# Kernel tuning notes

Hardware: AMD Instinct MI355X
Metric: run time of the kernel (lower is better)

The kernel has to match this reference:

```python
import jax, jax.numpy as jnp
import numpy as np
import math

B, S, D, H = 4, 2048, 1024, 16
HD = D // H  # head_dim = 64


def setup_inputs() -> dict:
    key = jax.random.key(0)
    ks = jax.random.split(key, 12)
    inv = 1.0 / math.sqrt(D)
    inp = {
        "query": jax.random.normal(ks[0], (B, S, D), dtype=jnp.float32),
        "key": jax.random.normal(ks[1], (B, S, D), dtype=jnp.float32),
        "value": jax.random.normal(ks[2], (B, S, D), dtype=jnp.float32),
        # causal mask, broadcast over heads; guarantees no all-masked softmax rows
        "mask": jnp.tril(jnp.ones((S, S), dtype=jnp.int32))[None, None].repeat(B, axis=0),
        # linear params stored as (in, out); y = x @ W + b (same math as torch Linear)
        "Wq": jax.random.uniform(ks[3], (D, D), jnp.float32, -inv, inv),
        "bq": jax.random.uniform(ks[4], (D,), jnp.float32, -inv, inv),
        "Wk": jax.random.uniform(ks[5], (D, D), jnp.float32, -inv, inv),
        "bk": jax.random.uniform(ks[6], (D,), jnp.float32, -inv, inv),
        "Wv": jax.random.uniform(ks[7], (D, D), jnp.float32, -inv, inv),
        "bv": jax.random.uniform(ks[8], (D,), jnp.float32, -inv, inv),
        "Wo": jax.random.uniform(ks[9], (D, D), jnp.float32, -inv, inv),
        "bo": jax.random.uniform(ks[10], (D,), jnp.float32, -inv, inv),
    }
    return inp


def _split_heads(x):
    # [B, S, D] -> [B, H, S, HD]
    b, s, _ = x.shape
    return x.reshape(b, s, H, HD).transpose(0, 2, 1, 3)


def reference(query, key, value, mask, Wq, bq, Wk, bk, Wv, bv, Wo, bo):
    q = _split_heads(query @ Wq + bq)   # [B,H,S,HD]
    k = _split_heads(key @ Wk + bk)
    v = _split_heads(value @ Wv + bv)
    scores = jnp.einsum("bhqd,bhkd->bhqk", q, k)          # [B,H,S,S]
    scores = jnp.where(mask == 0, -jnp.inf, scores)
    attn = jax.nn.softmax(scores / math.sqrt(HD), axis=-1)
    attn = attn * mask.astype(attn.dtype)                  # post-softmax re-mask (as in source)
    out = jnp.einsum("bhqk,bhkd->bhqd", attn, v)           # [B,H,S,HD]
    out = out.transpose(0, 2, 1, 3).reshape(query.shape[0], -1, D)
    return out @ Wo + bo
```

## Files before the change

### kernel.cpp

```cpp
#include <hip/hip_runtime.h>

typedef __attribute__((ext_vector_type(8))) short short8;
typedef __attribute__((ext_vector_type(8))) unsigned short ushort8;
typedef __attribute__((ext_vector_type(4))) unsigned short us4;
typedef __attribute__((ext_vector_type(4))) float f32x4;
typedef __attribute__((ext_vector_type(4))) int i32x4;

#define S_LEN 2048
#define D_MODEL 1024
#define N_HEADS 16
#define HEAD_DIM 64

__device__ __forceinline__ unsigned short f2bf(float f) {
  union { float f; unsigned u; } x; x.f = f;
  unsigned r = x.u + 0x7FFFu + ((x.u >> 16) & 1u);
  return (unsigned short)(r >> 16);
}

__device__ __forceinline__ int pkbf(float a, float b) {
  union { float f; unsigned u; } x, y;
  x.f = a; y.f = b;
  return (int)__builtin_amdgcn_perm(y.u + 0x8000u, x.u + 0x8000u, 0x07060302u);
}

__global__ __launch_bounds__(256) void cvt3_kernel(const float* __restrict__ a,
                                                   const float* __restrict__ b,
                                                   const float* __restrict__ c,
                                                   unsigned short* __restrict__ oa,
                                                   unsigned short* __restrict__ ob,
                                                   unsigned short* __restrict__ oc) {
  int bid = blockIdx.x;
  const float* in = (bid < 4096) ? a : (bid < 8192 ? b : c);
  unsigned short* out = (bid < 4096) ? oa : (bid < 8192 ? ob : oc);
  int i = (bid & 4095) * 256 + threadIdx.x;
  const f32x4* in4 = (const f32x4*)in;
  f32x4 x = in4[2 * i], y = in4[2 * i + 1];
  i32x4 o;
  o[0] = pkbf(x[0], x[1]);
  o[1] = pkbf(x[2], x[3]);
  o[2] = pkbf(y[0], y[1]);
  o[3] = pkbf(y[2], y[3]);
  ((i32x4*)out)[i] = o;
}

__global__ __launch_bounds__(256) void transpose_w4(
    const float* __restrict__ Wq, const float* __restrict__ Wk,
    const float* __restrict__ Wv, const float* __restrict__ Wo,
    unsigned short* __restrict__ wqkvT, unsigned short* __restrict__ woT) {
  __shared__ float tile[64][65];
  const int z = blockIdx.z;
  const float* W = (z == 0) ? Wq : (z == 1) ? Wk : (z == 2) ? Wv : Wo;
  unsigned short* Wt = (z < 3) ? (wqkvT + (size_t)z * D_MODEL * D_MODEL) : woT;
  const int no = blockIdx.x * 64, ko = blockIdx.y * 64;
  const int tx = threadIdx.x & 63, ty = threadIdx.x >> 6;
  for (int r = ty; r < 64; r += 4)
    tile[r][tx] = W[(size_t)(ko + r) * D_MODEL + no + tx];
  __syncthreads();
  for (int r = ty; r < 64; r += 4)
    Wt[(size_t)(no + r) * D_MODEL + ko + tx] = f2bf(tile[tx][r]);
}

template <int MODE>
__global__ __launch_bounds__(256) void proj_gemm(
    const unsigned short* __restrict__ A0,
    const unsigned short* __restrict__ A1,
    const unsigned short* __restrict__ A2,
    const unsigned short* __restrict__ Bt,
    const float* __restrict__ b0p, const float* __restrict__ b1p,
    const float* __restrict__ b2p,
    void* __restrict__ o0, void* __restrict__ o1, void* __restrict__ o2,
    float qscale) {
  __shared__ __align__(16) unsigned short sm[16384];
  unsigned short* As = sm;
  unsigned short* Bs = sm + 8192;
  const int tid = threadIdx.x;
  const int wave = tid >> 6, lane = tid & 63;
  const int quad = lane >> 4, l16 = lane & 15;

  const int nlin = blockIdx.y * (MODE == 0 ? 24 : 8) + blockIdx.x;
  const int xcd = nlin & 7;
  const int j = nlin >> 3;
  int bx_eff, by_eff;
  if (MODE == 0) {
    by_eff = xcd * 8 + ((j & 63) >> 3);
    bx_eff = (j >> 6) * 8 + (j & 7);
  } else {
    by_eff = xcd * 8 + (j >> 3);
    bx_eff = j & 7;
  }
  const int m0 = by_eff * 128, n0 = bx_eff * 128;
  const int wm = (wave >> 1) * 64, wn = (wave & 1) * 64;

  const int sel = (MODE == 0) ? (n0 >> 10) : 0;
  const unsigned short* A = (MODE == 0) ? (sel == 0 ? A0 : sel == 1 ? A1 : A2) : A0;
  const float* bias = (MODE == 0) ? (sel == 0 ? b0p : sel == 1 ? b1p : b2p) : b0p;
  const float scale = (MODE == 0 && sel == 0) ? qscale : 1.0f;
  const int nb = (MODE == 0) ? (n0 & 1023) : n0;

  f32x4 acc[4][4] = {};

  int grow[4], gcol[4];
  for (int i = 0; i < 4; ++i) {
    int cid = (wave * 4 + i) * 64 + lane;
    int r = cid >> 3;
    grow[i] = r;
    gcol[i] = ((cid & 7) ^ (r & 7)) * 8;
  }

  for (int k0 = 0; k0 < D_MODEL; k0 += 64) {
#pragma unroll
    for (int i = 0; i < 4; ++i) {
      const unsigned short* g = A + (size_t)(m0 + grow[i]) * D_MODEL + k0 + gcol[i];
      __builtin_amdgcn_global_load_lds((const __attribute__((address_space(1))) void*)g,
          (__attribute__((address_space(3))) void*)(As + (wave * 4 + i) * 512), 16, 0, 0);
    }
#pragma unroll
    for (int i = 0; i < 4; ++i) {
      const unsigned short* g = Bt + (size_t)(n0 + grow[i]) * D_MODEL + k0 + gcol[i];
      __builtin_amdgcn_global_load_lds((const __attribute__((address_space(1))) void*)g,
          (__attribute__((address_space(3))) void*)(Bs + (wave * 4 + i) * 512), 16, 0, 0);
    }
    __syncthreads();
#pragma unroll
    for (int t = 0; t < 2; ++t) {
      short8 af[4], bf[4];
#pragma unroll
      for (int i = 0; i < 4; ++i) {
        int r = wm + i * 16 + l16;
        af[i] = *(const short8*)(As + r * 64 + (((t * 4 + quad) ^ (r & 7)) << 3));
      }
#pragma unroll
      for (int j2 = 0; j2 < 4; ++j2) {
        int r = wn + j2 * 16 + l16;
        bf[j2] = *(const short8*)(Bs + r * 64 + (((t * 4 + quad) ^ (r & 7)) << 3));
      }
#pragma unroll
      for (int i = 0; i < 4; ++i)
#pragma unroll
        for (int j2 = 0; j2 < 4; ++j2)
          acc[i][j2] = __builtin_amdgcn_mfma_f32_16x16x32_bf16(af[i], bf[j2], acc[i][j2], 0, 0, 0);
    }
    __syncthreads();
  }

  float bv4[4];
#pragma unroll
  for (int j2 = 0; j2 < 4; ++j2) bv4[j2] = bias[nb + wn + j2 * 16 + l16];

  if (MODE == 0) {
    if (sel < 2) {
      unsigned short* T = As + wave * 1152;
      unsigned short* out = (unsigned short*)(sel == 0 ? o0 : o1);
      const int h = (nb + wn) >> 6;
#pragma unroll
      for (int i = 0; i < 4; ++i) {
#pragma unroll
        for (int j2 = 0; j2 < 4; ++j2)
#pragma unroll
          for (int r = 0; r < 4; ++r)
            T[(quad * 4 + r) * 72 + j2 * 16 + l16] = f2bf((acc[i][j2][r] + bv4[j2]) * scale);
        int m = m0 + wm + i * 16 + l16;
        int b = m >> 11, s = m & 2047;
#pragma unroll
        for (int t = 0; t < 2; ++t) {
          short8 row = *(const short8*)(T + l16 * 72 + t * 32 + quad * 8);
          *(short8*)(out + (((size_t)(b * N_HEADS + h) * S_LEN + s) << 6) + t * 32 + quad * 8) = row;
        }
      }
    } else {
      unsigned short* vt = (unsigned short*)o2;
#pragma unroll
      for (int i = 0; i < 4; ++i) {
        int m = m0 + wm + i * 16 + quad * 4;
        int b = m >> 11, s = m & 2047;
#pragma unroll
        for (int j2 = 0; j2 < 4; ++j2) {
          int n = nb + wn + j2 * 16 + l16;
          int h = n >> 6, d = n & 63;
          us4 pv;
#pragma unroll
          for (int r = 0; r < 4; ++r) pv[r] = f2bf(acc[i][j2][r] + bv4[j2]);
          *(us4*)(vt + (((size_t)(b * N_HEADS + h) * 64 + d) << 11) + s) = pv;
        }
      }
    }
  } else {
    float* Tf = (float*)sm + wave * 1088;
    float* out = (float*)o0;
#pragma unroll
    for (int i = 0; i < 4; ++i) {
#pragma unroll
      for (int j2 = 0; j2 < 4; ++j2)
#pragma unroll
        for (int r = 0; r < 4; ++r)
          Tf[(quad * 4 + r) * 68 + j2 * 16 + l16] = acc[i][j2][r] + bv4[j2];
      int m = m0 + wm + i * 16 + l16;
#pragma unroll
      for (int t = 0; t < 4; ++t) {
        f32x4 row = *(const f32x4*)(Tf + l16 * 68 + t * 16 + quad * 4);
        *(f32x4*)(out + (size_t)m * D_MODEL + nb + wn + t * 16 + quad * 4) = row;
      }
    }
  }
}

__global__ __launch_bounds__(256, 4) void flash_attn(
    const unsigned short* __restrict__ Qh,
    const unsigned short* __restrict__ Kh,
    const unsigned short* __restrict__ Vt,
    unsigned short* __restrict__ ctx) {
  __shared__ __align__(16) unsigned short smem[16384];
  const int tid = threadIdx.x;
  const int wave = tid >> 6, lane = tid & 63;
  const int quad = lane >> 4, l16 = lane & 15;
  const int l7 = l16 & 7;

  const int nlin = blockIdx.y * 16 + blockIdx.x;
  const int xcd = nlin & 7;
  const int rr = nlin >> 3;
  const int bh = xcd * 8 + (rr & 7);
  const int qslot = rr >> 3;
  const int qa = qslot & 3, qb = qslot >> 2;
  const int qbase = qa + ((qb >> 1) << 2);
  const int qi = (qb & 1) ? (15 - qbase) : qbase;
  const int q0 = qi * 128;
  const int nk = 2 * qi + 2;
  const size_t hb = (size_t)bh * (S_LEN * HEAD_DIM);
  const int srow = lane >> 3;
  const int schunk = ((lane & 7) ^ srow) * 8;

  auto stage = [&](int kt, int buf) {
    unsigned short* Kb = smem + buf * 8192;
    unsigned short* Vb = smem + buf * 8192 + 4096;
#pragma unroll
    for (int c = 0; c < 2; ++c) {
      int row = wave * 16 + c * 8 + srow;
      const unsigned short* gk = Kh + hb + (size_t)(kt * 64 + row) * 64 + schunk;
      __builtin_amdgcn_global_load_lds((const __attribute__((address_space(1))) void*)gk,
          (__attribute__((address_space(3))) void*)(Kb + (wave * 16 + c * 8) * 64), 16, 0, 0);
      const unsigned short* gv = Vt + hb + (size_t)row * S_LEN + kt * 64 + schunk;
      __builtin_amdgcn_global_load_lds((const __attribute__((address_space(1))) void*)gv,
          (__attribute__((address_space(3))) void*)(Vb + (wave * 16 + c * 8) * 64), 16, 0, 0);
    }
  };

  stage(0, 0);

  short8 qf[2][2];
#pragma unroll
  for (int s = 0; s < 2; ++s)
#pragma unroll
    for (int t = 0; t < 2; ++t)
      qf[s][t] = *(const short8*)(Qh + hb +
          (size_t)(q0 + wave * 32 + s * 16 + l16) * 64 + t * 32 + quad * 8);

  f32x4 o[4][2] = {};
  float rsum[2] = {0.f, 0.f};

  for (int kt = 0; kt < nk; ++kt) {
    __syncthreads();
    if (kt + 1 < nk) stage(kt + 1, (kt + 1) & 1);
    const unsigned short* Kb = smem + (kt & 1) * 8192;
    const unsigned short* Vb = Kb + 4096;

    if (kt * 64 > q0 + wave * 32 + 31) continue;

    f32x4 sc[2][4];
    __builtin_amdgcn_s_setprio(1);
#pragma unroll
    for (int nt = 0; nt < 4; ++nt) {
      short8 k0 = *(const short8*)(Kb + (nt * 16 + l16) * 64 + ((quad ^ l7) << 3));
      short8 k1 = *(const short8*)(Kb + (nt * 16 + l16) * 64 + (((4 + quad) ^ l7) << 3));
#pragma unroll
      for (int s = 0; s < 2; ++s) {
        f32x4 z = {};
        z = __builtin_amdgcn_mfma_f32_16x16x32_bf16(k0, qf[s][0], z, 0, 0, 0);
        sc[s][nt] = __builtin_amdgcn_mfma_f32_16x16x32_bf16(k1, qf[s][1], z, 0, 0, 0);
      }
    }
    __builtin_amdgcn_s_setprio(0);
    if (kt >= 2 * qi) {
#pragma unroll
      for (int s = 0; s < 2; ++s) {
        int qg = q0 + wave * 32 + s * 16 + l16;
#pragma unroll
        for (int nt = 0; nt < 4; ++nt) {
          int kg = kt * 64 + nt * 16 + quad * 4;
#pragma unroll
          for (int r = 0; r < 4; ++r)
            if (kg + r > qg) sc[s][nt][r] = -1e30f;
        }
      }
    }

    union { int i[4]; short8 v; } pf[2][2];
#pragma unroll
    for (int s = 0; s < 2; ++s) {
      int pk[4][2];
#pragma unroll
      for (int nt = 0; nt < 4; ++nt) {
        float p0 = __builtin_amdgcn_exp2f(sc[s][nt][0]);
        float p1 = __builtin_amdgcn_exp2f(sc[s][nt][1]);
        float p2 = __builtin_amdgcn_exp2f(sc[s][nt][2]);
        float p3 = __builtin_amdgcn_exp2f(sc[s][nt][3]);
        rsum[s] += (p0 + p1) + (p2 + p3);
        pk[nt][0] = pkbf(p0, p1);
        pk[nt][1] = pkbf(p2, p3);
      }
#pragma unroll
      for (int t = 0; t < 2; ++t) {
        int A = pk[t * 2][0], C = pk[t * 2 + 1][0];
        int B2 = pk[t * 2][1], D = pk[t * 2 + 1][1];
        asm("v_permlane32_swap_b32 %0, %1" : "+v"(A), "+v"(C));
        asm("v_permlane16_swap_b32 %0, %1" : "+v"(A), "+v"(C));
        asm("v_permlane32_swap_b32 %0, %1" : "+v"(B2), "+v"(D));
        asm("v_permlane16_swap_b32 %0, %1" : "+v"(B2), "+v"(D));
        pf[s][t].i[0] = A;
        pf[s][t].i[1] = B2;
        pf[s][t].i[2] = C;
        pf[s][t].i[3] = D;
      }
    }

    __builtin_amdgcn_s_setprio(1);
#pragma unroll
    for (int ntd = 0; ntd < 4; ++ntd) {
      short8 v0 = *(const short8*)(Vb + (ntd * 16 + l16) * 64 + ((quad ^ l7) << 3));
      short8 v1 = *(const short8*)(Vb + (ntd * 16 + l16) * 64 + (((4 + quad) ^ l7) << 3));
#pragma unroll
      for (int s = 0; s < 2; ++s) {
        o[ntd][s] = __builtin_amdgcn_mfma_f32_16x16x32_bf16(v0, pf[s][0].v, o[ntd][s], 0, 0, 0);
        o[ntd][s] = __builtin_amdgcn_mfma_f32_16x16x32_bf16(v1, pf[s][1].v, o[ntd][s], 0, 0, 0);
      }
    }
    __builtin_amdgcn_s_setprio(0);
  }

#pragma unroll
  for (int s = 0; s < 2; ++s) {
    rsum[s] += __shfl_xor(rsum[s], 16, 64);
    rsum[s] += __shfl_xor(rsum[s], 32, 64);
  }

  __syncthreads();
  unsigned short* Os = smem;
#pragma unroll
  for (int s = 0; s < 2; ++s) {
    float invl = 1.0f / rsum[s];
#pragma unroll
    for (int ntd = 0; ntd < 4; ++ntd) {
      us4 pk4;
#pragma unroll
      for (int r = 0; r < 4; ++r) pk4[r] = f2bf(o[ntd][s][r] * invl);
      *(us4*)(Os + (wave * 32 + s * 16 + l16) * 72 + ntd * 16 + quad * 4) = pk4;
    }
  }
  __syncthreads();
  const int b = bh >> 4, h = bh & 15;
#pragma unroll
  for (int it = 0; it < 4; ++it) {
    int e = it * 256 + tid;
    int row = e >> 3, c = (e & 7) * 8;
    short8 vrow = *(const short8*)(Os + row * 72 + c);
    *(short8*)(ctx + (size_t)(b * S_LEN + q0 + row) * D_MODEL + h * HEAD_DIM + c) = vrow;
  }
}

extern "C" void kernel_launch(void* const* d_in, const int* in_sizes, int n_in,
                              void* d_out, int out_size, void* d_ws, size_t ws_size,
                              hipStream_t stream) {
  (void)in_sizes; (void)n_in; (void)out_size;
  const float* q  = (const float*)d_in[0];
  const float* k  = (const float*)d_in[1];
  const float* v  = (const float*)d_in[2];
  const float* Wq = (const float*)d_in[4];
  const float* bq = (const float*)d_in[5];
  const float* Wk = (const float*)d_in[6];
  const float* bk = (const float*)d_in[7];
  const float* Wv = (const float*)d_in[8];
  const float* bv = (const float*)d_in[9];
  const float* Wo = (const float*)d_in[10];
  const float* bo = (const float*)d_in[11];
  float* out = (float*)d_out;

  if (ws_size < 109051904u) return;
  char* ws = (char*)d_ws;
  unsigned short* xq    = (unsigned short*)(ws);
  unsigned short* xk    = (unsigned short*)(ws + 16777216);
  unsigned short* xv    = (unsigned short*)(ws + 33554432);
  unsigned short* wqkvT = (unsigned short*)(ws + 50331648);
  unsigned short* woT   = (unsigned short*)(ws + 56623104);
  unsigned short* qh    = (unsigned short*)(ws + 58720256);
  unsigned short* kh    = qh + 8388608;
  unsigned short* vt    = kh + 8388608;
  unsigned short* ctx   = xq;

  cvt3_kernel<<<12288, 256, 0, stream>>>(q, k, v, xq, xk, xv);
  transpose_w4<<<dim3(16, 16, 4), 256, 0, stream>>>(Wq, Wk, Wv, Wo, wqkvT, woT);
  proj_gemm<0><<<dim3(24, 64), 256, 0, stream>>>(xq, xk, xv, wqkvT, bq, bk, bv,
                                                 qh, kh, vt, 0.125f * 1.44269504088896f);
  flash_attn<<<dim3(16, 64), 256, 0, stream>>>(qh, kh, vt, ctx);
  proj_gemm<1><<<dim3(8, 64), 256, 0, stream>>>(ctx, ctx, ctx, woT, bo, bo, bo,
                                                out, out, out, 1.0f);
}
```

Before: 328.9 us.

## Triple-buffer projection GEMM with 256x128 tiles and 512-thread blocks

Restructures the projection GEMM to use 256x128 output tiles computed by 8 waves, with a three-stage LDS ring in dynamic shared memory. Global-to-LDS loads run two k-steps ahead and are gated by vmcnt waits and raw s_barriers instead of __syncthreads. MFMA sections run at raised wave priority. This is meant to hide global load latency behind MFMA work and to increase reuse of the B tile. In exchange it needs 144KB of LDS, so only one block fits per CU. The hand-tuned wait and barrier placement may not fully synchronise other waves' loads before the next buffer is read.

```diff
diff --git a/kernel.cpp b/kernel.cpp
--- a/kernel.cpp
+++ b/kernel.cpp
@@ -61,7 +61,7 @@
 }
 
 template <int MODE>
-__global__ __launch_bounds__(256) void proj_gemm(
+__global__ __launch_bounds__(512) void proj_gemm(
     const unsigned short* __restrict__ A0,
     const unsigned short* __restrict__ A1,
     const unsigned short* __restrict__ A2,
@@ -70,9 +70,7 @@
     const float* __restrict__ b2p,
     void* __restrict__ o0, void* __restrict__ o1, void* __restrict__ o2,
     float qscale) {
-  __shared__ __align__(16) unsigned short sm[16384];
-  unsigned short* As = sm;
-  unsigned short* Bs = sm + 8192;
+  extern __shared__ __align__(16) unsigned short smem_d[];
   const int tid = threadIdx.x;
   const int wave = tid >> 6, lane = tid & 63;
   const int quad = lane >> 4, l16 = lane & 15;
@@ -82,13 +80,13 @@
   const int j = nlin >> 3;
   int bx_eff, by_eff;
   if (MODE == 0) {
-    by_eff = xcd * 8 + ((j & 63) >> 3);
-    bx_eff = (j >> 6) * 8 + (j & 7);
+    by_eff = xcd * 4 + ((j >> 3) & 3);
+    bx_eff = (j >> 5) * 8 + (j & 7);
   } else {
-    by_eff = xcd * 8 + (j >> 3);
+    by_eff = xcd * 4 + (j >> 3);
     bx_eff = j & 7;
   }
-  const int m0 = by_eff * 128, n0 = bx_eff * 128;
+  const int m0 = by_eff * 256, n0 = bx_eff * 128;
   const int wm = (wave >> 1) * 64, wn = (wave & 1) * 64;
 
   const int sel = (MODE == 0) ? (n0 >> 10) : 0;
@@ -99,48 +97,61 @@
 
   f32x4 acc[4][4] = {};
 
-  int grow[4], gcol[4];
-  for (int i = 0; i < 4; ++i) {
-    int cid = (wave * 4 + i) * 64 + lane;
-    int r = cid >> 3;
-    grow[i] = r;
-    gcol[i] = ((cid & 7) ^ (r & 7)) * 8;
-  }
-
-  for (int k0 = 0; k0 < D_MODEL; k0 += 64) {
-#pragma unroll
-    for (int i = 0; i < 4; ++i) {
-      const unsigned short* g = A + (size_t)(m0 + grow[i]) * D_MODEL + k0 + gcol[i];
+  const int srw = wave * 8 + (lane >> 3);
+  const int sch = ((lane & 7) ^ ((lane >> 3) & 7)) << 3;
+
+  auto stage = [&](int kt, int half) {
+    unsigned short* Ab = smem_d + (kt % 3) * 24576;
+    unsigned short* Bb = Ab + 16384;
+    const int k0 = kt * 64;
+#pragma unroll
+    for (int rr = 0; rr < 2; ++rr) {
+      const int rd = half * 2 + rr;
+      const unsigned short* g = A + (size_t)(m0 + rd * 64 + srw) * D_MODEL + k0 + sch;
       __builtin_amdgcn_global_load_lds((const __attribute__((address_space(1))) void*)g,
-          (__attribute__((address_space(3))) void*)(As + (wave * 4 + i) * 512), 16, 0, 0);
-    }
-#pragma unroll
-    for (int i = 0; i < 4; ++i) {
-      const unsigned short* g = Bt + (size_t)(n0 + grow[i]) * D_MODEL + k0 + gcol[i];
-      __builtin_amdgcn_global_load_lds((const __attribute__((address_space(1))) void*)g,
-          (__attribute__((address_space(3))) void*)(Bs + (wave * 4 + i) * 512), 16, 0, 0);
-    }
-    __syncthreads();
+          (__attribute__((address_space(3))) void*)(Ab + rd * 4096 + wave * 512), 16, 0, 0);
+    }
+    const unsigned short* gb = Bt + (size_t)(n0 + half * 64 + srw) * D_MODEL + k0 + sch;
+    __builtin_amdgcn_global_load_lds((const __attribute__((address_space(1))) void*)gb,
+        (__attribute__((address_space(3))) void*)(Bb + half * 4096 + wave * 512), 16, 0, 0);
+  };
+
+  stage(0, 0); stage(0, 1); stage(1, 0); stage(1, 1);
+  asm volatile("s_waitcnt vmcnt(6)" ::: "memory");
+  __builtin_amdgcn_s_barrier();
+
+  for (int kt = 0; kt < 16; ++kt) {
+    const unsigned short* Ab = smem_d + (kt % 3) * 24576;
+    const unsigned short* Bb = Ab + 16384;
 #pragma unroll
     for (int t = 0; t < 2; ++t) {
+      if (kt + 2 < 16) stage(kt + 2, t);
       short8 af[4], bf[4];
 #pragma unroll
       for (int i = 0; i < 4; ++i) {
         int r = wm + i * 16 + l16;
-        af[i] = *(const short8*)(As + r * 64 + (((t * 4 + quad) ^ (r & 7)) << 3));
+        af[i] = *(const short8*)(Ab + r * 64 + (((t * 4 + quad) ^ (r & 7)) << 3));
       }
 #pragma unroll
       for (int j2 = 0; j2 < 4; ++j2) {
         int r = wn + j2 * 16 + l16;
-        bf[j2] = *(const short8*)(Bs + r * 64 + (((t * 4 + quad) ^ (r & 7)) << 3));
-      }
+        bf[j2] = *(const short8*)(Bb + r * 64 + (((t * 4 + quad) ^ (r & 7)) << 3));
+      }
+      __builtin_amdgcn_s_barrier();
+      __builtin_amdgcn_s_setprio(1);
 #pragma unroll
       for (int i = 0; i < 4; ++i)
 #pragma unroll
         for (int j2 = 0; j2 < 4; ++j2)
           acc[i][j2] = __builtin_amdgcn_mfma_f32_16x16x32_bf16(af[i], bf[j2], acc[i][j2], 0, 0, 0);
-    }
-    __syncthreads();
+      __builtin_amdgcn_s_setprio(0);
+      __builtin_amdgcn_s_barrier();
+    }
+    if (kt + 2 < 16) {
+      asm volatile("s_waitcnt vmcnt(6)" ::: "memory");
+    } else {
+      asm volatile("s_waitcnt vmcnt(0)" ::: "memory");
+    }
   }
 
   float bv4[4];
@@ -149,7 +160,7 @@
 
   if (MODE == 0) {
     if (sel < 2) {
-      unsigned short* T = As + wave * 1152;
+      unsigned short* T = smem_d + wave * 1152;
       unsigned short* out = (unsigned short*)(sel == 0 ? o0 : o1);
       const int h = (nb + wn) >> 6;
 #pragma unroll
@@ -185,7 +196,7 @@
       }
     }
   } else {
-    float* Tf = (float*)sm + wave * 1088;
+    float* Tf = (float*)smem_d + wave * 1088;
     float* out = (float*)o0;
 #pragma unroll
     for (int i = 0; i < 4; ++i) {
@@ -395,11 +406,22 @@
   unsigned short* vt    = kh + 8388608;
   unsigned short* ctx   = xq;
 
+  static int attr_done = 0;
+  if (!attr_done) {
+    auto* k0f = proj_gemm<0>;
+    auto* k1f = proj_gemm<1>;
+    hipFuncSetAttribute(reinterpret_cast<const void*>(k0f),
+                        hipFuncAttributeMaxDynamicSharedMemorySize, 147456);
+    hipFuncSetAttribute(reinterpret_cast<const void*>(k1f),
+                        hipFuncAttributeMaxDynamicSharedMemorySize, 147456);
+    attr_done = 1;
+  }
+
   cvt3_kernel<<<12288, 256, 0, stream>>>(q, k, v, xq, xk, xv);
   transpose_w4<<<dim3(16, 16, 4), 256, 0, stream>>>(Wq, Wk, Wv, Wo, wqkvT, woT);
-  proj_gemm<0><<<dim3(24, 64), 256, 0, stream>>>(xq, xk, xv, wqkvT, bq, bk, bv,
-                                                 qh, kh, vt, 0.125f * 1.44269504088896f);
+  proj_gemm<0><<<dim3(24, 32), 512, 147456, stream>>>(xq, xk, xv, wqkvT, bq, bk, bv,
+                                                      qh, kh, vt, 0.125f * 1.44269504088896f);
   flash_attn<<<dim3(16, 64), 256, 0, stream>>>(qh, kh, vt, ctx);
-  proj_gemm<1><<<dim3(8, 64), 256, 0, stream>>>(ctx, ctx, ctx, woT, bo, bo, bo,
-                                                out, out, out, 1.0f);
-}
+  proj_gemm<1><<<dim3(8, 32), 512, 147456, stream>>>(ctx, ctx, ctx, woT, bo, bo, bo,
+                                                     out, out, out, 1.0f);
+}
```

Measured after the change: 322.2 us. 1.02x faster.
